# Performance work log

Hardware: AMD Instinct MI355X
Metric: run time of the kernel (lower is better)

Reference implementation:

```python
import jax, jax.numpy as jnp
import numpy as np

NEG_SLOPE = 0.2  # PyG GATConv default negative_slope
EPS = 1e-16      # PyG softmax denominator eps


def gat_layer(x, src, dst, W, a_src, a_dst, num_nodes):
    """One GATConv (eval mode, self-loops already appended to src/dst).
    x: [N, Fin], W: [Fin, H*C], a_src/a_dst: [H, C]. Returns [N, H, C]."""
    H, C = a_src.shape
    h = (x @ W).reshape(num_nodes, H, C)                  # [N,H,C]
    alpha_src = jnp.sum(h * a_src, axis=-1)               # [N,H]
    alpha_dst = jnp.sum(h * a_dst, axis=-1)               # [N,H]
    e = alpha_src[src] + alpha_dst[dst]                   # [E,H]
    e = jnp.where(e > 0, e, NEG_SLOPE * e)                # leaky_relu
    # segment softmax keyed by destination node
    m = jax.ops.segment_max(e, dst, num_segments=num_nodes)   # [N,H]
    ex = jnp.exp(e - m[dst])                              # [E,H]
    s = jax.ops.segment_sum(ex, dst, num_segments=num_nodes)  # [N,H]
    alpha = ex / (s[dst] + EPS)                           # [E,H]
    # weighted scatter-aggregation of source features
    msg = h[src] * alpha[..., None]                       # [E,H,C]
    out = jax.ops.segment_sum(msg, dst, num_segments=num_nodes)  # [N,H,C]
    return out


def setup_inputs() -> dict:
    key = jax.random.key(0)
    ks = jax.random.split(key, 10)
    N, E = 50000, 800000
    Fin, C1, H, Fout = 128, 32, 8, 1
    x = jax.random.normal(ks[0], (N, Fin), dtype=jnp.float32)
    edge_index = jax.random.randint(ks[1], (2, E), 0, N).astype(jnp.int64)
    sc = 0.1
    W1 = jax.random.normal(ks[2], (Fin, H * C1), dtype=jnp.float32) * sc
    att_src1 = jax.random.normal(ks[3], (H, C1), dtype=jnp.float32) * sc
    att_dst1 = jax.random.normal(ks[4], (H, C1), dtype=jnp.float32) * sc
    bias1 = jnp.zeros((H * C1,), dtype=jnp.float32)
    W2 = jax.random.normal(ks[5], (H * C1, Fout), dtype=jnp.float32) * sc
    att_src2 = jax.random.normal(ks[6], (1, Fout), dtype=jnp.float32) * sc
    att_dst2 = jax.random.normal(ks[7], (1, Fout), dtype=jnp.float32) * sc
    bias2 = jnp.zeros((Fout,), dtype=jnp.float32)
    return {"x": x, "edge_index": edge_index, "W1": W1, "att_src1": att_src1,
            "att_dst1": att_dst1, "bias1": bias1, "W2": W2, "att_src2": att_src2,
            "att_dst2": att_dst2, "bias2": bias2}


def reference(x, edge_index, W1, att_src1, att_dst1, bias1, W2, att_src2, att_dst2, bias2):
    N = x.shape[0]
    loops = jnp.arange(N, dtype=edge_index.dtype)
    src = jnp.concatenate([edge_index[0], loops])   # add_self_loops=True
    dst = jnp.concatenate([edge_index[1], loops])
    # layer 1: heads=8, concat=True
    h1 = gat_layer(x, src, dst, W1, att_src1, att_dst1, N)      # [N,H,C1]
    h1 = h1.reshape(N, -1) + bias1                               # [N,H*C1]
    h1 = jax.nn.elu(h1)
    # layer 2: heads=1, concat=False (single head -> identity mean)
    h2 = gat_layer(h1, src, dst, W2, att_src2, att_dst2, N)      # [N,1,1]
    h2 = h2.reshape(N, -1) + bias2                               # [N,1]
    return jax.nn.sigmoid(h2).squeeze(-1)                        # [N]
```

## Files before the change

### kernel.cpp

```cpp
#include <hip/hip_runtime.h>
#include <math.h>

#define NEG_SLOPE 0.2f
#define GAT_EPS 1e-16f
#define NEG_BIG -3.0e38f
#define MAXDEG 96
#define H1STRIDE 288
#define BCAP 6144
#define CHUNK 2048

typedef __attribute__((ext_vector_type(8))) short short8;
typedef __attribute__((ext_vector_type(4))) float floatx4;

__device__ __forceinline__ float leaky(float v) {
    return v > 0.f ? v : NEG_SLOPE * v;
}
__device__ __forceinline__ unsigned short f2bf(float f) {
    unsigned u = __float_as_uint(f);
    unsigned r = u + 0x7FFFu + ((u >> 16) & 1u);
    return (unsigned short)(r >> 16);
}
__device__ __forceinline__ float bf2f(unsigned short h) {
    return __uint_as_float(((unsigned)h) << 16);
}

__global__ void prep_kernel(const float* __restrict__ W1,
    const float* __restrict__ a_src, const float* __restrict__ a_dst,
    unsigned short* __restrict__ w1t)
{
    int idx = blockIdx.x * blockDim.x + threadIdx.x;
    if (idx < 128 * 256) {
        int n = idx >> 7, k = idx & 127;
        w1t[idx] = f2bf(W1[(size_t)k * 256 + n]);
    }
    if (idx < 2048) {
        int j = idx >> 7, k = idx & 127;
        const float* a = (j < 8) ? (a_src + j * 32) : (a_dst + (j - 8) * 32);
        const float* wr = W1 + (size_t)k * 256 + (j & 7) * 32;
        float s = 0.f;
        #pragma unroll
        for (int c = 0; c < 32; ++c) s += wr[c] * a[c];
        w1t[(size_t)(256 + j) * 128 + k] = f2bf(s);
    }
}

__global__ __launch_bounds__(256) void scatter_passA(
    const int* __restrict__ ei, unsigned int* __restrict__ bucket_buf,
    int* __restrict__ bucket_cnt, int E, int ET)
{
    __shared__ int lhist[256];
    __shared__ int lbase[256];
    const int t = threadIdx.x;
    lhist[t] = 0;
    __syncthreads();
    const int base = blockIdx.x * CHUNK;
    unsigned int pk[8]; int bk[8], rk[8]; bool v[8];
    #pragma unroll
    for (int k = 0; k < 8; ++k) {
        int i = base + k * 256 + t;
        v[k] = i < ET;
        int ii = v[k] ? i : 0;
        int src = (ii < E) ? ei[ii] : (ii - E);
        int dst = (ii < E) ? ei[E + ii] : (ii - E);
        bk[k] = dst >> 8;
        pk[k] = ((unsigned)src << 8) | (unsigned)(dst & 255);
    }
    #pragma unroll
    for (int k = 0; k < 8; ++k)
        if (v[k]) rk[k] = atomicAdd(&lhist[bk[k]], 1);
    __syncthreads();
    if (lhist[t] > 0) lbase[t] = atomicAdd(&bucket_cnt[t], lhist[t]);
    __syncthreads();
    #pragma unroll
    for (int k = 0; k < 8; ++k) {
        if (v[k]) {
            int pos = lbase[bk[k]] + rk[k];
            if (pos < BCAP) bucket_buf[(size_t)bk[k] * BCAP + pos] = pk[k];
        }
    }
}

__global__ __launch_bounds__(256) void scatter_passB(
    const unsigned int* __restrict__ bucket_buf, const int* __restrict__ bucket_cnt,
    int* __restrict__ cnt, unsigned short* __restrict__ csr_pad, int N)
{
    __shared__ int lcnt[256];
    const int b = blockIdx.x;
    const int t = threadIdx.x;
    lcnt[t] = 0;
    __syncthreads();
    int tot = bucket_cnt[b]; if (tot > BCAP) tot = BCAP;
    const unsigned int* bp = bucket_buf + (size_t)b * BCAP;
    for (int j = t; j < tot; j += 256) {
        unsigned int e = bp[j];
        int loc = e & 255;
        int src = (int)(e >> 8);
        int slot = atomicAdd(&lcnt[loc], 1);
        if (slot < MAXDEG)
            csr_pad[(((size_t)b << 8) | loc) * MAXDEG + slot] = (unsigned short)src;
    }
    __syncthreads();
    int node = (b << 8) | t;
    if (node < N) cnt[node] = lcnt[t];
}

__global__ __launch_bounds__(256) void gemm1_kernel(
    const float* __restrict__ x, const unsigned short* __restrict__ w1t,
    unsigned short* __restrict__ h1b, float* __restrict__ ad1, int N)
{
    __shared__ __align__(16) unsigned short Asl[64][40];
    __shared__ __align__(16) unsigned short Bsl[272][40];
    const int t = threadIdx.x;
    const int row0 = blockIdx.x * 64;
    const int wave = t >> 6, lane = t & 63;
    const int l15 = lane & 15, quad = lane >> 4;

    floatx4 acc[17];
    #pragma unroll
    for (int i = 0; i < 17; ++i) acc[i] = (floatx4){0.f, 0.f, 0.f, 0.f};

    for (int kc = 0; kc < 128; kc += 32) {
        {
            int r = t >> 2, q = t & 3;
            int row = row0 + r; if (row > N - 1) row = N - 1;
            const float4* xp = (const float4*)(x + (size_t)row * 128 + kc + q * 8);
            float4 f0 = xp[0], f1 = xp[1];
            ushort4 u0, u1;
            u0.x = f2bf(f0.x); u0.y = f2bf(f0.y); u0.z = f2bf(f0.z); u0.w = f2bf(f0.w);
            u1.x = f2bf(f1.x); u1.y = f2bf(f1.y); u1.z = f2bf(f1.z); u1.w = f2bf(f1.w);
            *(ushort4*)&Asl[r][q * 8] = u0;
            *(ushort4*)&Asl[r][q * 8 + 4] = u1;
        }
        {
            #pragma unroll
            for (int q = 0; q < 4; ++q) {
                uint4 v = *(const uint4*)&w1t[(size_t)t * 128 + kc + q * 8];
                *(uint4*)&Bsl[t][q * 8] = v;
            }
            if (t < 16) {
                #pragma unroll
                for (int q = 0; q < 4; ++q) {
                    uint4 v = *(const uint4*)&w1t[(size_t)(256 + t) * 128 + kc + q * 8];
                    *(uint4*)&Bsl[256 + t][q * 8] = v;
                }
            }
        }
        __syncthreads();
        short8 a = *(const short8*)&Asl[wave * 16 + l15][quad * 8];
        #pragma unroll
        for (int nt = 0; nt < 17; ++nt) {
            short8 bb = *(const short8*)&Bsl[nt * 16 + l15][quad * 8];
            acc[nt] = __builtin_amdgcn_mfma_f32_16x16x32_bf16(a, bb, acc[nt], 0, 0, 0);
        }
        __syncthreads();
    }
    #pragma unroll
    for (int reg = 0; reg < 4; ++reg) {
        int row = row0 + wave * 16 + quad * 4 + reg;
        if (row < N) {
            unsigned short* rp = h1b + (size_t)row * H1STRIDE;
            #pragma unroll
            for (int nt = 0; nt < 16; ++nt)
                rp[nt * 16 + l15] = f2bf(acc[nt][reg]);
            float vv = acc[16][reg];
            if (l15 < 8) ((float*)(rp + 256))[l15] = vv;
            else         ad1[(size_t)row * 8 + l15 - 8] = vv;
        }
    }
}

__global__ __launch_bounds__(256) void aggr1_fused(
    const int* __restrict__ cnt, const unsigned short* __restrict__ csr_pad,
    const float* __restrict__ ad1,
    const unsigned short* __restrict__ h1b,
    const float* __restrict__ bias1, const float* __restrict__ W2,
    float* __restrict__ h2, int N)
{
    int n = blockIdx.x * 4 + (threadIdx.x >> 6);
    int lane = threadIdx.x & 63;
    if (n >= N) return;
    const size_t rs = (size_t)n * MAXDEG;
    int deg = cnt[n]; if (deg > MAXDEG) deg = MAXDEG;
    int le = lane >> 3, lh = lane & 7, hh = lane >> 3;
    float adv = ad1[(size_t)n * 8 + lh];

    float m = NEG_BIG, s = 0.f;
    float4 acc = make_float4(0.f, 0.f, 0.f, 0.f);

    for (int j0 = 0; j0 < deg; j0 += 8) {
        int sv = 0;
        if (lane < 8 && j0 + lane < deg) sv = csr_pad[rs + j0 + lane];
        int srcs[8];
        #pragma unroll
        for (int j = 0; j < 8; ++j) srcs[j] = __shfl(sv, j);
        float l = NEG_BIG;
        if (j0 + le < deg)
            l = leaky(((const float*)(h1b + (size_t)srcs[le] * H1STRIDE + 256))[lh] + adv);
        ushort4 hv[8];
        #pragma unroll
        for (int j = 0; j < 8; ++j)
            hv[j] = *(const ushort4*)&h1b[(size_t)srcs[j] * H1STRIDE + lane * 4];
        float lj[8];
        #pragma unroll
        for (int j = 0; j < 8; ++j) lj[j] = __shfl(l, (j << 3) | hh);
        float Mc = lj[0];
        #pragma unroll
        for (int j = 1; j < 8; ++j) Mc = fmaxf(Mc, lj[j]);
        float mn = fmaxf(m, Mc);
        float sc = __expf(m - mn);
        s *= sc;
        acc.x *= sc; acc.y *= sc; acc.z *= sc; acc.w *= sc;
        #pragma unroll
        for (int j = 0; j < 8; ++j) {
            float p = __expf(lj[j] - mn);
            s += p;
            acc.x += p * bf2f(hv[j].x); acc.y += p * bf2f(hv[j].y);
            acc.z += p * bf2f(hv[j].z); acc.w += p * bf2f(hv[j].w);
        }
        m = mn;
    }
    float inv = 1.f / (s + GAT_EPS);
    acc.x *= inv; acc.y *= inv; acc.z *= inv; acc.w *= inv;

    float4 b = *(const float4*)&bias1[lane * 4];
    acc.x += b.x; acc.y += b.y; acc.z += b.z; acc.w += b.w;
    acc.x = acc.x > 0.f ? acc.x : __expf(acc.x) - 1.f;
    acc.y = acc.y > 0.f ? acc.y : __expf(acc.y) - 1.f;
    acc.z = acc.z > 0.f ? acc.z : __expf(acc.z) - 1.f;
    acc.w = acc.w > 0.f ? acc.w : __expf(acc.w) - 1.f;
    float4 w = *(const float4*)&W2[lane * 4];
    float part = acc.x * w.x + acc.y * w.y + acc.z * w.z + acc.w * w.w;
    #pragma unroll
    for (int mask = 1; mask < 64; mask <<= 1) part += __shfl_xor(part, mask);
    if (lane == 0) h2[n] = part;
}

__global__ __launch_bounds__(256) void layer2_fused(
    const int* __restrict__ cnt, const unsigned short* __restrict__ csr_pad,
    const float* __restrict__ h2, const float* __restrict__ a_s2,
    const float* __restrict__ a_d2, const float* __restrict__ bias2,
    float* __restrict__ out, int N)
{
    int n = blockIdx.x * 16 + (threadIdx.x >> 4);
    int sl = threadIdx.x & 15;
    if (n >= N) return;
    const size_t rs = (size_t)n * MAXDEG;
    int deg = cnt[n]; if (deg > MAXDEG) deg = MAXDEG;
    float asc = a_s2[0], adc = a_d2[0];
    float hdc = h2[n] * adc;

    int k0 = sl, k1 = sl + 16;
    float hs0 = 0.f, hs1 = 0.f;
    bool v0 = k0 < deg, v1 = k1 < deg;
    if (v0) hs0 = h2[csr_pad[rs + k0]];
    if (v1) hs1 = h2[csr_pad[rs + k1]];

    float m = NEG_BIG, s = 0.f;
    if (v0) { m = leaky(hs0 * asc + hdc); s = 1.f; }
    if (v1) {
        float l = leaky(hs1 * asc + hdc);
        if (l > m) { s = s * __expf(m - l) + 1.f; m = l; }
        else       { s += __expf(l - m); }
    }
    for (int k = sl + 32; k < deg; k += 16) {
        float hs = h2[csr_pad[rs + k]];
        float l = leaky(hs * asc + hdc);
        if (l > m) { s = s * __expf(m - l) + 1.f; m = l; }
        else       { s += __expf(l - m); }
    }
    #pragma unroll
    for (int mask = 1; mask < 16; mask <<= 1) {
        float mo = __shfl_xor(m, mask);
        float so = __shfl_xor(s, mask);
        float M = fmaxf(m, mo);
        s = s * __expf(m - M) + so * __expf(mo - M);
        m = M;
    }
    float inv = 1.f / (s + GAT_EPS);

    float acc = 0.f;
    if (v0) acc += __expf(leaky(hs0 * asc + hdc) - m) * hs0;
    if (v1) acc += __expf(leaky(hs1 * asc + hdc) - m) * hs1;
    for (int k = sl + 32; k < deg; k += 16) {
        float hs = h2[csr_pad[rs + k]];
        float l = leaky(hs * asc + hdc);
        acc += __expf(l - m) * hs;
    }
    #pragma unroll
    for (int mask = 1; mask < 16; mask <<= 1) acc += __shfl_xor(acc, mask);
    if (sl == 0) {
        float z = acc * inv + bias2[0];
        out[n] = 1.f / (1.f + __expf(-z));
    }
}

extern "C" void kernel_launch(void* const* d_in, const int* in_sizes, int n_in,
                              void* d_out, int out_size, void* d_ws, size_t ws_size,
                              hipStream_t stream)
{
    const float* x      = (const float*)d_in[0];
    const int*   ei     = (const int*)  d_in[1];
    const float* W1     = (const float*)d_in[2];
    const float* a_src1 = (const float*)d_in[3];
    const float* a_dst1 = (const float*)d_in[4];
    const float* bias1  = (const float*)d_in[5];
    const float* W2     = (const float*)d_in[6];
    const float* a_s2   = (const float*)d_in[7];
    const float* a_d2   = (const float*)d_in[8];
    const float* bias2  = (const float*)d_in[9];
    float* out = (float*)d_out;

    const int N  = in_sizes[0] / 128;
    const int E  = in_sizes[1] / 2;
    const int ET = E + N;
    const int ntiles   = (N + 63) / 64;
    const int nbuckets = (N + 255) >> 8;
    const int ablocks  = (ET + CHUNK - 1) / CHUNK;

    char* wsb = (char*)d_ws;
    size_t off = 0;
    auto walloc = [&](size_t bytes) -> void* {
        void* p = wsb + off;
        off += (bytes + 255) & ~(size_t)255;
        return p;
    };
    unsigned short* w1t     = (unsigned short*)walloc((size_t)272 * 128 * 2);
    unsigned short* h1b     = (unsigned short*)walloc((size_t)N * H1STRIDE * 2);
    float*          ad1     = (float*)         walloc((size_t)N * 8 * 4);
    float*          h2      = (float*)         walloc((size_t)N * 4);
    int*            cnt     = (int*)           walloc((size_t)N * 4);
    unsigned short* csr_pad = (unsigned short*)walloc((size_t)N * MAXDEG * 2);
    int*            bucket_cnt = (int*)        walloc(256 * 4);
    unsigned int*   bucket_buf = (unsigned int*)h1b;

    hipMemsetAsync(bucket_cnt, 0, 256 * sizeof(int), stream);

    prep_kernel<<<136, 256, 0, stream>>>(W1, a_src1, a_dst1, w1t);

    scatter_passA<<<ablocks, 256, 0, stream>>>(ei, bucket_buf, bucket_cnt, E, ET);
    scatter_passB<<<nbuckets, 256, 0, stream>>>(bucket_buf, bucket_cnt, cnt, csr_pad, N);

    gemm1_kernel<<<ntiles, 256, 0, stream>>>(x, w1t, h1b, ad1, N);

    aggr1_fused<<<(N + 3) / 4, 256, 0, stream>>>(cnt, csr_pad, ad1, h1b,
                                                 bias1, W2, h2, N);
    layer2_fused<<<(N + 15) / 16, 256, 0, stream>>>(cnt, csr_pad, h2,
                                                    a_s2, a_d2, bias2, out, N);
}
```

Measured before the change: 207.3 us.

## Merge prep/scatter/gemm launches, split attention logits, lazy-rescale softmax with exp2

The prep kernel is folded into scatter pass A and scatter pass B into the GEMM kernel via block-index dispatch, cutting two launches and letting independent work overlap. The source attention logits move to a separate [N,8] array, so h1 rows become exactly 256 bf16 (512 B aligned) and the bucket buffer gets its own allocation instead of aliasing h1b. Aggregation preloads up to 128 CSR indices per node with two loads instead of reloading each chunk. It uses exp2 with pre-scaled logits and only rescales the running max when a new max exceeds it by more than 8. The cost is extra workspace and slightly more register use in the fused kernels.

```diff
diff --git a/kernel.cpp b/kernel.cpp
--- a/kernel.cpp
+++ b/kernel.cpp
@@ -4,10 +4,11 @@
 #define NEG_SLOPE 0.2f
 #define GAT_EPS 1e-16f
 #define NEG_BIG -3.0e38f
+#define LOG2E 1.4426950408889634f
 #define MAXDEG 96
-#define H1STRIDE 288
 #define BCAP 6144
 #define CHUNK 2048
+#define PREPB 136
 
 typedef __attribute__((ext_vector_type(8))) short short8;
 typedef __attribute__((ext_vector_type(4))) float floatx4;
@@ -24,36 +25,37 @@
     return __uint_as_float(((unsigned)h) << 16);
 }
 
-__global__ void prep_kernel(const float* __restrict__ W1,
-    const float* __restrict__ a_src, const float* __restrict__ a_dst,
-    unsigned short* __restrict__ w1t)
-{
-    int idx = blockIdx.x * blockDim.x + threadIdx.x;
-    if (idx < 128 * 256) {
-        int n = idx >> 7, k = idx & 127;
-        w1t[idx] = f2bf(W1[(size_t)k * 256 + n]);
-    }
-    if (idx < 2048) {
-        int j = idx >> 7, k = idx & 127;
-        const float* a = (j < 8) ? (a_src + j * 32) : (a_dst + (j - 8) * 32);
-        const float* wr = W1 + (size_t)k * 256 + (j & 7) * 32;
-        float s = 0.f;
-        #pragma unroll
-        for (int c = 0; c < 32; ++c) s += wr[c] * a[c];
-        w1t[(size_t)(256 + j) * 128 + k] = f2bf(s);
-    }
-}
-
-__global__ __launch_bounds__(256) void scatter_passA(
+__global__ __launch_bounds__(256) void prep_scatterA(
+    const float* __restrict__ W1, const float* __restrict__ a_src,
+    const float* __restrict__ a_dst, unsigned short* __restrict__ w1t,
     const int* __restrict__ ei, unsigned int* __restrict__ bucket_buf,
     int* __restrict__ bucket_cnt, int E, int ET)
 {
     __shared__ int lhist[256];
     __shared__ int lbase[256];
     const int t = threadIdx.x;
+
+    if (blockIdx.x < PREPB) {
+        int idx = blockIdx.x * 256 + t;
+        if (idx < 128 * 256) {
+            int n = idx >> 7, k = idx & 127;
+            w1t[idx] = f2bf(W1[(size_t)k * 256 + n]);
+        }
+        if (idx < 2048) {
+            int j = idx >> 7, k = idx & 127;
+            const float* a = (j < 8) ? (a_src + j * 32) : (a_dst + (j - 8) * 32);
+            const float* wr = W1 + (size_t)k * 256 + (j & 7) * 32;
+            float s = 0.f;
+            #pragma unroll
+            for (int c = 0; c < 32; ++c) s += wr[c] * a[c];
+            w1t[(size_t)(256 + j) * 128 + k] = f2bf(s);
+        }
+        return;
+    }
+
     lhist[t] = 0;
     __syncthreads();
-    const int base = blockIdx.x * CHUNK;
+    const int base = (blockIdx.x - PREPB) * CHUNK;
     unsigned int pk[8]; int bk[8], rk[8]; bool v[8];
     #pragma unroll
     for (int k = 0; k < 8; ++k) {
@@ -80,37 +82,38 @@
     }
 }
 
-__global__ __launch_bounds__(256) void scatter_passB(
+__global__ __launch_bounds__(256) void gemm_scatterB(
+    const float* __restrict__ x, const unsigned short* __restrict__ w1t,
+    unsigned short* __restrict__ h1b, float* __restrict__ as1, float* __restrict__ ad1,
     const unsigned int* __restrict__ bucket_buf, const int* __restrict__ bucket_cnt,
-    int* __restrict__ cnt, unsigned short* __restrict__ csr_pad, int N)
-{
-    __shared__ int lcnt[256];
-    const int b = blockIdx.x;
-    const int t = threadIdx.x;
-    lcnt[t] = 0;
-    __syncthreads();
-    int tot = bucket_cnt[b]; if (tot > BCAP) tot = BCAP;
-    const unsigned int* bp = bucket_buf + (size_t)b * BCAP;
-    for (int j = t; j < tot; j += 256) {
-        unsigned int e = bp[j];
-        int loc = e & 255;
-        int src = (int)(e >> 8);
-        int slot = atomicAdd(&lcnt[loc], 1);
-        if (slot < MAXDEG)
-            csr_pad[(((size_t)b << 8) | loc) * MAXDEG + slot] = (unsigned short)src;
-    }
-    __syncthreads();
-    int node = (b << 8) | t;
-    if (node < N) cnt[node] = lcnt[t];
-}
-
-__global__ __launch_bounds__(256) void gemm1_kernel(
-    const float* __restrict__ x, const unsigned short* __restrict__ w1t,
-    unsigned short* __restrict__ h1b, float* __restrict__ ad1, int N)
+    int* __restrict__ cnt, unsigned short* __restrict__ csr_pad,
+    int N, int ntiles)
 {
     __shared__ __align__(16) unsigned short Asl[64][40];
     __shared__ __align__(16) unsigned short Bsl[272][40];
+    __shared__ int lcnt[256];
     const int t = threadIdx.x;
+
+    if (blockIdx.x >= ntiles) {
+        const int b = blockIdx.x - ntiles;
+        lcnt[t] = 0;
+        __syncthreads();
+        int tot = bucket_cnt[b]; if (tot > BCAP) tot = BCAP;
+        const unsigned int* bp = bucket_buf + (size_t)b * BCAP;
+        for (int j = t; j < tot; j += 256) {
+            unsigned int e = bp[j];
+            int loc = e & 255;
+            int src = (int)(e >> 8);
+            int slot = atomicAdd(&lcnt[loc], 1);
+            if (slot < MAXDEG)
+                csr_pad[(((size_t)b << 8) | loc) * MAXDEG + slot] = (unsigned short)src;
+        }
+        __syncthreads();
+        int node = (b << 8) | t;
+        if (node < N) cnt[node] = lcnt[t];
+        return;
+    }
+
     const int row0 = blockIdx.x * 64;
     const int wave = t >> 6, lane = t & 63;
     const int l15 = lane & 15, quad = lane >> 4;
@@ -158,12 +161,12 @@
     for (int reg = 0; reg < 4; ++reg) {
         int row = row0 + wave * 16 + quad * 4 + reg;
         if (row < N) {
-            unsigned short* rp = h1b + (size_t)row * H1STRIDE;
+            unsigned short* rp = h1b + ((size_t)row << 8);
             #pragma unroll
             for (int nt = 0; nt < 16; ++nt)
                 rp[nt * 16 + l15] = f2bf(acc[nt][reg]);
-            float vv = acc[16][reg];
-            if (l15 < 8) ((float*)(rp + 256))[l15] = vv;
+            float vv = acc[16][reg] * LOG2E;
+            if (l15 < 8) as1[(size_t)row * 8 + l15] = vv;
             else         ad1[(size_t)row * 8 + l15 - 8] = vv;
         }
     }
@@ -171,7 +174,7 @@
 
 __global__ __launch_bounds__(256) void aggr1_fused(
     const int* __restrict__ cnt, const unsigned short* __restrict__ csr_pad,
-    const float* __restrict__ ad1,
+    const float* __restrict__ as1, const float* __restrict__ ad1,
     const unsigned short* __restrict__ h1b,
     const float* __restrict__ bias1, const float* __restrict__ W2,
     float* __restrict__ h2, int N)
@@ -184,41 +187,48 @@
     int le = lane >> 3, lh = lane & 7, hh = lane >> 3;
     float adv = ad1[(size_t)n * 8 + lh];
 
+    int c0 = 0, c1 = 0;
+    if (lane < deg)      c0 = csr_pad[rs + lane];
+    if (64 + lane < deg) c1 = csr_pad[rs + 64 + lane];
+
     float m = NEG_BIG, s = 0.f;
     float4 acc = make_float4(0.f, 0.f, 0.f, 0.f);
 
     for (int j0 = 0; j0 < deg; j0 += 8) {
-        int sv = 0;
-        if (lane < 8 && j0 + lane < deg) sv = csr_pad[rs + j0 + lane];
+        int cc = (j0 < 64) ? c0 : c1;
+        int bo = j0 & 63;
         int srcs[8];
         #pragma unroll
-        for (int j = 0; j < 8; ++j) srcs[j] = __shfl(sv, j);
-        float l = NEG_BIG;
-        if (j0 + le < deg)
-            l = leaky(((const float*)(h1b + (size_t)srcs[le] * H1STRIDE + 256))[lh] + adv);
-        ushort4 hv[8];
+        for (int j = 0; j < 8; ++j) srcs[j] = __shfl(cc, bo + j);
+        uint2 hv[8];
         #pragma unroll
         for (int j = 0; j < 8; ++j)
-            hv[j] = *(const ushort4*)&h1b[(size_t)srcs[j] * H1STRIDE + lane * 4];
+            hv[j] = *(const uint2*)&h1b[((size_t)srcs[j] << 8) + lane * 4];
+        float av = as1[(size_t)srcs[le] * 8 + lh];
+        float l = (j0 + le < deg) ? leaky(av + adv) : NEG_BIG;
         float lj[8];
         #pragma unroll
         for (int j = 0; j < 8; ++j) lj[j] = __shfl(l, (j << 3) | hh);
-        float Mc = lj[0];
-        #pragma unroll
-        for (int j = 1; j < 8; ++j) Mc = fmaxf(Mc, lj[j]);
-        float mn = fmaxf(m, Mc);
-        float sc = __expf(m - mn);
-        s *= sc;
-        acc.x *= sc; acc.y *= sc; acc.z *= sc; acc.w *= sc;
+        float Mc = fmaxf(fmaxf(fmaxf(lj[0], lj[1]), fmaxf(lj[2], lj[3])),
+                         fmaxf(fmaxf(lj[4], lj[5]), fmaxf(lj[6], lj[7])));
+        if (__any(Mc > m + 8.f)) {
+            float mn = fmaxf(m, Mc);
+            float sc = exp2f(m - mn);
+            s *= sc; acc.x *= sc; acc.y *= sc; acc.z *= sc; acc.w *= sc;
+            m = mn;
+        }
         #pragma unroll
         for (int j = 0; j < 8; ++j) {
-            float p = __expf(lj[j] - mn);
+            float p = exp2f(lj[j] - m);
             s += p;
-            acc.x += p * bf2f(hv[j].x); acc.y += p * bf2f(hv[j].y);
-            acc.z += p * bf2f(hv[j].z); acc.w += p * bf2f(hv[j].w);
-        }
-        m = mn;
-    }
+            unsigned d0 = hv[j].x, d1 = hv[j].y;
+            acc.x += p * __uint_as_float(d0 << 16);
+            acc.y += p * __uint_as_float(d0 & 0xFFFF0000u);
+            acc.z += p * __uint_as_float(d1 << 16);
+            acc.w += p * __uint_as_float(d1 & 0xFFFF0000u);
+        }
+    }
+
     float inv = 1.f / (s + GAT_EPS);
     acc.x *= inv; acc.y *= inv; acc.z *= inv; acc.w *= inv;
 
@@ -325,24 +335,25 @@
         return p;
     };
     unsigned short* w1t     = (unsigned short*)walloc((size_t)272 * 128 * 2);
-    unsigned short* h1b     = (unsigned short*)walloc((size_t)N * H1STRIDE * 2);
+    unsigned short* h1b     = (unsigned short*)walloc((size_t)N * 256 * 2);
+    float*          as1     = (float*)         walloc((size_t)N * 8 * 4);
     float*          ad1     = (float*)         walloc((size_t)N * 8 * 4);
     float*          h2      = (float*)         walloc((size_t)N * 4);
     int*            cnt     = (int*)           walloc((size_t)N * 4);
     unsigned short* csr_pad = (unsigned short*)walloc((size_t)N * MAXDEG * 2);
     int*            bucket_cnt = (int*)        walloc(256 * 4);
-    unsigned int*   bucket_buf = (unsigned int*)h1b;
+    unsigned int*   bucket_buf = (unsigned int*)walloc((size_t)nbuckets * BCAP * 4);
 
     hipMemsetAsync(bucket_cnt, 0, 256 * sizeof(int), stream);
 
-    prep_kernel<<<136, 256, 0, stream>>>(W1, a_src1, a_dst1, w1t);
-
-    scatter_passA<<<ablocks, 256, 0, stream>>>(ei, bucket_buf, bucket_cnt, E, ET);
-    scatter_passB<<<nbuckets, 256, 0, stream>>>(bucket_buf, bucket_cnt, cnt, csr_pad, N);
-
-    gemm1_kernel<<<ntiles, 256, 0, stream>>>(x, w1t, h1b, ad1, N);
-
-    aggr1_fused<<<(N + 3) / 4, 256, 0, stream>>>(cnt, csr_pad, ad1, h1b,
+    prep_scatterA<<<PREPB + ablocks, 256, 0, stream>>>(W1, a_src1, a_dst1, w1t,
+                                                       ei, bucket_buf, bucket_cnt, E, ET);
+
+    gemm_scatterB<<<ntiles + nbuckets, 256, 0, stream>>>(x, w1t, h1b, as1, ad1,
+                                                         bucket_buf, bucket_cnt,
+                                                         cnt, csr_pad, N, ntiles);
+
+    aggr1_fused<<<(N + 3) / 4, 256, 0, stream>>>(cnt, csr_pad, as1, ad1, h1b,
                                                  bias1, W2, h2, N);
     layer2_fused<<<(N + 15) / 16, 256, 0, stream>>>(cnt, csr_pad, h2,
                                                     a_s2, a_d2, bias2, out, N);
```

Measured after the change: 195.2 us. 1.06x faster.
